# Performance work log

Hardware: AMD Instinct MI355X
Metric: run time of the kernel (lower is better)

## Reference

```python
import jax, jax.numpy as jnp
import numpy as np

IMAGE_C = 1
IMAGE_W = 28
PIXELS_PER_ROW = IMAGE_W * IMAGE_C  # 28

B, T, E = 16, IMAGE_W * IMAGE_W * IMAGE_C, 512  # T = 784
H = 8
D = E // H  # head_dim = 64


def get_2d_causal_bias(T):
    idx = jnp.arange(T)
    i = idx // PIXELS_PER_ROW          # row index
    j = (idx % PIXELS_PER_ROW) // IMAGE_C  # col index
    c = idx % IMAGE_C                  # channel index
    q_i, k_i = i[:, None], i[None, :]
    q_j, k_j = j[:, None], j[None, :]
    q_c, k_c = c[:, None], c[None, :]
    allowed = (k_i < q_i) | ((k_i == q_i) & (k_j < q_j)) | (
        (k_i == q_i) & (k_j == q_j) & (k_c <= q_c))
    bias = jnp.where(allowed, 0.0, -jnp.inf).astype(jnp.float32)
    return bias[None, None]  # [1, 1, T, T]


def setup_inputs() -> dict:
    key = jax.random.key(0)
    ks = jax.random.split(key, 5)
    s = 1.0 / np.sqrt(E)
    return {
        "x": jax.random.normal(ks[0], (B, T, E), dtype=jnp.float32),
        "Wq": jax.random.normal(ks[1], (E, E), dtype=jnp.float32) * s,
        "bq": jnp.zeros((E,), dtype=jnp.float32),
        "Wk": jax.random.normal(ks[2], (E, E), dtype=jnp.float32) * s,
        "bk": jnp.zeros((E,), dtype=jnp.float32),
        "Wv": jax.random.normal(ks[3], (E, E), dtype=jnp.float32) * s,
        "bv": jnp.zeros((E,), dtype=jnp.float32),
        "Wo": jax.random.normal(ks[4], (E, E), dtype=jnp.float32) * s,
        "bo": jnp.zeros((E,), dtype=jnp.float32),
    }


def reference(x, Wq, bq, Wk, bk, Wv, bv, Wo, bo):
    Bx, Tx, Ex = x.shape
    # projections (torch Linear: y = x @ W.T + b; here W stored as [E, E] used directly)
    Q = (x @ Wq + bq).reshape(Bx, Tx, H, D).transpose(0, 2, 1, 3)  # [B,H,T,D]
    K = (x @ Wk + bk).reshape(Bx, Tx, H, D).transpose(0, 2, 1, 3)
    V = (x @ Wv + bv).reshape(Bx, Tx, H, D).transpose(0, 2, 1, 3)
    scores = jnp.einsum("bhqd,bhkd->bhqk", Q, K) / jnp.sqrt(jnp.float32(D))
    scores = scores + get_2d_causal_bias(Tx)
    attn = jax.nn.softmax(scores, axis=-1)
    ctx = jnp.einsum("bhqk,bhkd->bhqd", attn, V)
    ctx = ctx.transpose(0, 2, 1, 3).reshape(Bx, Tx, Ex)
    return ctx @ Wo + bo
```

## Files before the change

### kernel.cpp

```cpp
#include <hip/hip_runtime.h>
#include <hip/hip_bf16.h>

#define BB    16
#define TT    784
#define TP    832
#define EE    512
#define HH    8
#define DD    64
#define BT    (BB*TT)

typedef short short8 __attribute__((ext_vector_type(8)));
typedef short short4v __attribute__((ext_vector_type(4)));
typedef float floatx4 __attribute__((ext_vector_type(4)));

__device__ __forceinline__ short f2bf(float f) {
    unsigned u = __builtin_bit_cast(unsigned, f);
    u += 0x7FFFu + ((u >> 16) & 1u);
    return (short)(u >> 16);
}

#define ASYNC16(g, l) __builtin_amdgcn_global_load_lds( \
    (const __attribute__((address_space(1))) void*)(g), \
    (__attribute__((address_space(3))) void*)(l), 16, 0, 0)

__global__ void prep_kernel(const float* __restrict__ x, short* __restrict__ xb,
                            const float* __restrict__ Wq, const float* __restrict__ Wk,
                            const float* __restrict__ Wv, short* __restrict__ wqkvt,
                            const float* __restrict__ Wo, short* __restrict__ wot,
                            short* __restrict__ Qb, short* __restrict__ Kb, short* __restrict__ Vt)
{
    __shared__ short t[64][65];
    int b = blockIdx.x;
    if (b < 3136) {
        int i = (b * 256 + threadIdx.x) * 8;
        float4 a = *(const float4*)(x + i);
        float4 c = *(const float4*)(x + i + 4);
        short8 o;
        o[0] = f2bf(a.x); o[1] = f2bf(a.y); o[2] = f2bf(a.z); o[3] = f2bf(a.w);
        o[4] = f2bf(c.x); o[5] = f2bf(c.y); o[6] = f2bf(c.z); o[7] = f2bf(c.w);
        *(short8*)(xb + i) = o;
    } else if (b < 3392) {
        const float* W; short* out; int n0, k0;
        if (b < 3328) {
            int tt = b - 3136;
            n0 = (tt % 24) * 64; k0 = (tt / 24) * 64;
            W = (n0 < 512) ? Wq : (n0 < 1024 ? Wk : Wv);
            out = wqkvt;
        } else {
            int tt = b - 3328;
            n0 = (tt % 8) * 64; k0 = (tt / 8) * 64;
            W = Wo; out = wot;
        }
        int nn0 = n0 & 511;
        for (int i = threadIdx.x; i < 4096; i += 256) {
            int r = i >> 6, c = i & 63;
            t[r][c] = f2bf(W[(k0 + r) * 512 + nn0 + c]);
        }
        __syncthreads();
        for (int i = threadIdx.x; i < 4096; i += 256) {
            int nr = i >> 6, kc = i & 63;
            out[(n0 + nr) * 512 + k0 + kc] = t[kc][nr];
        }
    } else {
        int idx = (b - 3392) * 256 + threadIdx.x;
        int d = idx & 63;
        int r = (idx >> 6) % 48;
        int bh = idx / (48 * 64);
        int off = (bh * TP + TT + r) * 64 + d;
        Qb[off] = 0; Kb[off] = 0;
        int c = idx % 48;
        int rest = idx / 48;
        int dv = rest & 63, bhv = rest >> 6;
        Vt[(bhv * 64 + dv) * TP + TT + c] = 0;
    }
}

__global__ __launch_bounds__(256, 4) void gemm_qkv_kernel(
    const short* __restrict__ A, const short* __restrict__ Bt,
    const float* __restrict__ bq, const float* __restrict__ bk, const float* __restrict__ bv,
    short* __restrict__ Qb, short* __restrict__ Kb, short* __restrict__ Vt)
{
    __shared__ __align__(16) short smem[16640];
    short* As0 = smem;
    short* Bs0 = smem + 8192;

    const int m0 = blockIdx.x * 128, n0 = blockIdx.y * 128;
    const int tid = threadIdx.x;
    const int lane = tid & 63, w = tid >> 6;
    const int wr = w >> 1, wc = w & 1;
    const int l16 = lane & 15, quad = lane >> 4;

    const short* Ag = A  + (size_t)(m0 + w * 32 + (lane >> 2)) * 512 + (lane & 3) * 8;
    const short* Bg = Bt + (size_t)(n0 + w * 32 + (lane >> 2)) * 512 + (lane & 3) * 8;
    short* Asw = As0 + (w * 32) * 32;
    short* Bsw = Bs0 + (w * 32) * 32;

    floatx4 acc[4][4];
    #pragma unroll
    for (int i = 0; i < 4; i++)
        #pragma unroll
        for (int j = 0; j < 4; j++)
            acc[i][j] = (floatx4){0.f, 0.f, 0.f, 0.f};

    ASYNC16(Ag, Asw);
    ASYNC16(Ag + 16 * 512, Asw + 16 * 32);
    ASYNC16(Bg, Bsw);
    ASYNC16(Bg + 16 * 512, Bsw + 16 * 32);

    for (int it = 0; it < 16; it++) {
        __syncthreads();
        if (it < 15) {
            int nb = (it + 1) & 1;
            int ko = (it + 1) * 32;
            ASYNC16(Ag + ko,            Asw + nb * 4096);
            ASYNC16(Ag + ko + 16 * 512, Asw + nb * 4096 + 16 * 32);
            ASYNC16(Bg + ko,            Bsw + nb * 4096);
            ASYNC16(Bg + ko + 16 * 512, Bsw + nb * 4096 + 16 * 32);
        }
        const short* as = As0 + (it & 1) * 4096;
        const short* bs = Bs0 + (it & 1) * 4096;
        short8 af[4], bf[4];
        #pragma unroll
        for (int i = 0; i < 4; i++) {
            af[i] = *(const short8*)&as[(wr * 64 + i * 16 + l16) * 32 + quad * 8];
            bf[i] = *(const short8*)&bs[(wc * 64 + i * 16 + l16) * 32 + quad * 8];
        }
        #pragma unroll
        for (int mi = 0; mi < 4; mi++)
            #pragma unroll
            for (int ni = 0; ni < 4; ni++)
                acc[mi][ni] = __builtin_amdgcn_mfma_f32_16x16x32_bf16(af[mi], bf[ni], acc[mi][ni], 0, 0, 0);
    }

    __syncthreads();

    short* Ct = smem;
    const int sel = n0 >> 9;
    const float* bias = (sel == 0) ? bq : (sel == 1) ? bk : bv;
    #pragma unroll
    for (int mi = 0; mi < 4; mi++) {
        #pragma unroll
        for (int ni = 0; ni < 4; ni++) {
            int nl = wc * 64 + ni * 16 + l16;
            int nn = (n0 + nl) & 511;
            float b = bias[nn];
            #pragma unroll
            for (int r = 0; r < 4; r++) {
                float v = acc[mi][ni][r] + b;
                if (sel == 0) v *= 0.125f;
                Ct[(wr * 64 + mi * 16 + quad * 4 + r) * 130 + nl] = f2bf(v);
            }
        }
    }
    __syncthreads();

    if (sel < 2) {
        short* dst = (sel == 0) ? Qb : Kb;
        int nl = lane * 2;
        int nn = (n0 + nl) & 511;
        int hh = nn >> 6, dd = nn & 63;
        #pragma unroll 4
        for (int rr = 0; rr < 32; rr++) {
            int ml = w * 32 + rr;
            int m = m0 + ml;
            int bb = m / TT, t = m - bb * TT;
            unsigned pv = *(const unsigned*)&Ct[ml * 130 + nl];
            *(unsigned*)&dst[((bb * HH + hh) * TP + t) * 64 + dd] = pv;
        }
    } else {
        #pragma unroll 4
        for (int rr = 0; rr < 32; rr++) {
            int nl = w * 32 + rr;
            int nn = (n0 + nl) & 511;
            int hh = nn >> 6, dd = nn & 63;
            #pragma unroll
            for (int j = 0; j < 2; j++) {
                int ml = j * 64 + lane;
                int m = m0 + ml;
                int bb = m / TT, t = m - bb * TT;
                Vt[((size_t)(bb * HH + hh) * 64 + dd) * TP + t] = Ct[ml * 130 + nl];
            }
        }
    }
}

#define LK 72
__global__ __launch_bounds__(256, 3) void attn_kernel(
    const short* __restrict__ Qb, const short* __restrict__ Kb, const short* __restrict__ Vt,
    short* __restrict__ ctx)
{
    const int g = blockIdx.x;
    const int low = g & 7, rest = g >> 3;
    const int qt = 12 - (rest >> 4);
    const int bh = ((rest & 15) << 3) | low;
    const int bb = bh >> 3, hh = bh & 7;
    const int tid = threadIdx.x;
    const int lane = tid & 63, w = tid >> 6;
    const int l16 = lane & 15, quad = lane >> 4;

    __shared__ short Ks[2][64 * LK];
    __shared__ short Vs[2][64 * LK];
    __shared__ short Ps[64 * LK];

    const int srow = tid >> 3;
    const int sc8 = (tid & 7) * 8;
    const short* Kbase = Kb + (size_t)(bh * TP) * 64;
    const short* Vbase = Vt + (size_t)(bh * 64) * TP;

    short8 kreg[2], vreg[2];
    auto load_tile = [&](int kt) {
        #pragma unroll
        for (int p = 0; p < 2; p++) {
            int row = srow + p * 32;
            kreg[p] = *(const short8*)(Kbase + (kt * 64 + row) * 64 + sc8);
            vreg[p] = *(const short8*)(Vbase + row * TP + kt * 64 + sc8);
        }
    };
    auto store_tile = [&](int b) {
        #pragma unroll
        for (int p = 0; p < 2; p++) {
            int row = srow + p * 32;
            *(short8*)&Ks[b][row * LK + sc8] = kreg[p];
            *(short8*)&Vs[b][row * LK + sc8] = vreg[p];
        }
    };

    const short* Qrow = Qb + (size_t)((bh * TP + qt * 64 + w * 16 + l16)) * 64;
    short8 qa0 = *(const short8*)(Qrow + quad * 8);
    short8 qa1 = *(const short8*)(Qrow + 32 + quad * 8);

    floatx4 accO[4];
    floatx4 accL = (floatx4){0.f, 0.f, 0.f, 0.f};
    #pragma unroll
    for (int dt = 0; dt < 4; dt++) accO[dt] = (floatx4){0.f, 0.f, 0.f, 0.f};

    short8 ones8;
    #pragma unroll
    for (int j = 0; j < 8; j++) ones8[j] = (short)0x3F80;

    const int pswz  = (quad >> 1) * 16;
    const int prswz = ((l16 >> 3) & 1) * 16;
    short* Pw = &Ps[(w * 16 + quad * 4) * LK];

    load_tile(0);
    store_tile(0);

    for (int kt = 0; kt <= qt; kt++) {
        const int cb = kt & 1;
        const bool diag = (kt == qt);
        if (kt < qt) load_tile(kt + 1);
        __syncthreads();

        float p[4][4];
        #pragma unroll
        for (int ni = 0; ni < 4; ni++) {
            if (diag && ni > w) {
                #pragma unroll
                for (int r = 0; r < 4; r++) p[ni][r] = 0.f;
                continue;
            }
            short8 kb0 = *(short8*)&Ks[cb][(ni * 16 + l16) * LK + quad * 8];
            short8 kb1 = *(short8*)&Ks[cb][(ni * 16 + l16) * LK + 32 + quad * 8];
            floatx4 z = (floatx4){0.f, 0.f, 0.f, 0.f};
            z = __builtin_amdgcn_mfma_f32_16x16x32_bf16(qa0, kb0, z, 0, 0, 0);
            z = __builtin_amdgcn_mfma_f32_16x16x32_bf16(qa1, kb1, z, 0, 0, 0);
            if (diag && ni == w) {
                #pragma unroll
                for (int r = 0; r < 4; r++)
                    if (l16 > quad * 4 + r) z[r] = -1e30f;
            }
            #pragma unroll
            for (int r = 0; r < 4; r++) p[ni][r] = __expf(z[r]);
        }

        #pragma unroll
        for (int ni = 0; ni < 4; ni++) {
            int col = (ni * 16 + l16) ^ pswz;
            #pragma unroll
            for (int r = 0; r < 4; r++)
                Pw[r * LK + col] = (short)(__builtin_bit_cast(unsigned, p[ni][r]) >> 16);
        }

        #pragma unroll
        for (int kk = 0; kk < 2; kk++) {
            if (diag && (kk * 32 > w * 16 + 15)) continue;
            short8 pa = *(short8*)&Ps[(w * 16 + l16) * LK + ((kk * 32 + quad * 8) ^ prswz)];
            accL = __builtin_amdgcn_mfma_f32_16x16x32_bf16(pa, ones8, accL, 0, 0, 0);
            #pragma unroll
            for (int dt = 0; dt < 4; dt++) {
                short8 vb = *(short8*)&Vs[cb][(dt * 16 + l16) * LK + kk * 32 + quad * 8];
                accO[dt] = __builtin_amdgcn_mfma_f32_16x16x32_bf16(pa, vb, accO[dt], 0, 0, 0);
            }
        }

        if (kt < qt) store_tile((kt + 1) & 1);
    }

    float inv_l[4];
    #pragma unroll
    for (int r = 0; r < 4; r++) inv_l[r] = 1.f / accL[r];
    #pragma unroll
    for (int dt = 0; dt < 4; dt++)
        #pragma unroll
        for (int r = 0; r < 4; r++) {
            int qg = qt * 64 + w * 16 + quad * 4 + r;
            if (qg < TT)
                ctx[(size_t)(bb * TT + qg) * 512 + hh * 64 + dt * 16 + l16] = f2bf(accO[dt][r] * inv_l[r]);
        }
}

__global__ __launch_bounds__(256, 4) void gemm_out_kernel(
    const short* __restrict__ A, const short* __restrict__ Bt,
    const float* __restrict__ bo, float* __restrict__ out)
{
    __shared__ __align__(16) short smem[16384];
    short* As0 = smem;
    short* Bs0 = smem + 8192;

    const int m0 = blockIdx.x * 128, n0 = blockIdx.y * 128;
    const int tid = threadIdx.x;
    const int lane = tid & 63, w = tid >> 6;
    const int wr = w >> 1, wc = w & 1;
    const int l16 = lane & 15, quad = lane >> 4;

    const short* Ag = A  + (size_t)(m0 + w * 32 + (lane >> 2)) * 512 + (lane & 3) * 8;
    const short* Bg = Bt + (size_t)(n0 + w * 32 + (lane >> 2)) * 512 + (lane & 3) * 8;
    short* Asw = As0 + (w * 32) * 32;
    short* Bsw = Bs0 + (w * 32) * 32;

    floatx4 acc[4][4];
    #pragma unroll
    for (int i = 0; i < 4; i++)
        #pragma unroll
        for (int j = 0; j < 4; j++)
            acc[i][j] = (floatx4){0.f, 0.f, 0.f, 0.f};

    ASYNC16(Ag, Asw);
    ASYNC16(Ag + 16 * 512, Asw + 16 * 32);
    ASYNC16(Bg, Bsw);
    ASYNC16(Bg + 16 * 512, Bsw + 16 * 32);

    for (int it = 0; it < 16; it++) {
        __syncthreads();
        if (it < 15) {
            int nb = (it + 1) & 1;
            int ko = (it + 1) * 32;
            ASYNC16(Ag + ko,            Asw + nb * 4096);
            ASYNC16(Ag + ko + 16 * 512, Asw + nb * 4096 + 16 * 32);
            ASYNC16(Bg + ko,            Bsw + nb * 4096);
            ASYNC16(Bg + ko + 16 * 512, Bsw + nb * 4096 + 16 * 32);
        }
        const short* as = As0 + (it & 1) * 4096;
        const short* bs = Bs0 + (it & 1) * 4096;
        short8 af[4], bf[4];
        #pragma unroll
        for (int i = 0; i < 4; i++) {
            af[i] = *(const short8*)&as[(wr * 64 + i * 16 + l16) * 32 + quad * 8];
            bf[i] = *(const short8*)&bs[(wc * 64 + i * 16 + l16) * 32 + quad * 8];
        }
        #pragma unroll
        for (int mi = 0; mi < 4; mi++)
            #pragma unroll
            for (int ni = 0; ni < 4; ni++)
                acc[mi][ni] = __builtin_amdgcn_mfma_f32_16x16x32_bf16(af[mi], bf[ni], acc[mi][ni], 0, 0, 0);
    }

    #pragma unroll
    for (int mi = 0; mi < 4; mi++) {
        #pragma unroll
        for (int ni = 0; ni < 4; ni++) {
            int n = n0 + wc * 64 + ni * 16 + l16;
            float bias = bo[n];
            #pragma unroll
            for (int r = 0; r < 4; r++) {
                int m = m0 + wr * 64 + mi * 16 + quad * 4 + r;
                out[(size_t)m * 512 + n] = acc[mi][ni][r] + bias;
            }
        }
    }
}

extern "C" void kernel_launch(void* const* d_in, const int* in_sizes, int n_in,
                              void* d_out, int out_size, void* d_ws, size_t ws_size,
                              hipStream_t stream) {
    const float* x  = (const float*)d_in[0];
    const float* Wq = (const float*)d_in[1];
    const float* bq = (const float*)d_in[2];
    const float* Wk = (const float*)d_in[3];
    const float* bk = (const float*)d_in[4];
    const float* Wv = (const float*)d_in[5];
    const float* bv = (const float*)d_in[6];
    const float* Wo = (const float*)d_in[7];
    const float* bo = (const float*)d_in[8];
    float* out = (float*)d_out;

    char* ws = (char*)d_ws;
    size_t off = 0;
    auto alloc = [&](size_t bytes) -> void* {
        void* p = ws + off;
        off += (bytes + 255) & ~(size_t)255;
        return p;
    };
    short* xb    = (short*)alloc((size_t)BT * EE * 2);
    short* wqkvt = (short*)alloc((size_t)1536 * 512 * 2);
    short* wot   = (short*)alloc((size_t)512 * 512 * 2);
    short* Qb    = (short*)alloc((size_t)BB * HH * TP * DD * 2);
    short* Kb    = (short*)alloc((size_t)BB * HH * TP * DD * 2);
    short* Vtb   = (short*)alloc((size_t)BB * HH * DD * TP * 2);
    short* ctxb  = (short*)alloc((size_t)BT * EE * 2);

    prep_kernel<<<4928, 256, 0, stream>>>(x, xb, Wq, Wk, Wv, wqkvt, Wo, wot, Qb, Kb, Vtb);
    gemm_qkv_kernel<<<dim3(98, 12), 256, 0, stream>>>(xb, wqkvt, bq, bk, bv, Qb, Kb, Vtb);
    attn_kernel<<<1664, 256, 0, stream>>>(Qb, Kb, Vtb, ctxb);
    gemm_out_kernel<<<dim3(98, 4), 256, 0, stream>>>(ctxb, wot, bo, out);
}
```

Measured before the change: 169.0 us.

## Use 128-row query tiles in attention and write V directly from registers

```diff
diff --git a/kernel.cpp b/kernel.cpp
--- a/kernel.cpp
+++ b/kernel.cpp
@@ -3,7 +3,8 @@
 
 #define BB    16
 #define TT    784
-#define TP    832
+#define TPK   832
+#define TPQ   896
 #define EE    512
 #define HH    8
 #define DD    64
@@ -62,16 +63,21 @@
             out[(n0 + nr) * 512 + k0 + kc] = t[kc][nr];
         }
     } else {
-        int idx = (b - 3392) * 256 + threadIdx.x;
-        int d = idx & 63;
-        int r = (idx >> 6) % 48;
-        int bh = idx / (48 * 64);
-        int off = (bh * TP + TT + r) * 64 + d;
-        Qb[off] = 0; Kb[off] = 0;
-        int c = idx % 48;
-        int rest = idx / 48;
-        int dv = rest & 63, bhv = rest >> 6;
-        Vt[(bhv * 64 + dv) * TP + TT + c] = 0;
+        int c = (b - 3392) * 256 + threadIdx.x;
+        short8 z = (short8){0,0,0,0,0,0,0,0};
+        if (c < 114688) {
+            int bh = c / 896, j = c - bh * 896;
+            *(short8*)&Qb[(bh * TPQ + TT) * 64 + j * 8] = z;
+        } else if (c < 163840) {
+            int c2 = c - 114688;
+            int bh = c2 / 384, j = c2 - bh * 384;
+            *(short8*)&Kb[(bh * TPK + TT) * 64 + j * 8] = z;
+        } else {
+            int c3 = c - 163840;
+            int bh = c3 / 384, j = c3 - bh * 384;
+            int d = j / 6, m = j - d * 6;
+            *(short8*)&Vt[(bh * 64 + d) * TPK + TT + m * 8] = z;
+        }
     }
 }
 
@@ -132,30 +138,29 @@
                 acc[mi][ni] = __builtin_amdgcn_mfma_f32_16x16x32_bf16(af[mi], bf[ni], acc[mi][ni], 0, 0, 0);
     }
 
-    __syncthreads();
-
-    short* Ct = smem;
     const int sel = n0 >> 9;
-    const float* bias = (sel == 0) ? bq : (sel == 1) ? bk : bv;
-    #pragma unroll
-    for (int mi = 0; mi < 4; mi++) {
-        #pragma unroll
-        for (int ni = 0; ni < 4; ni++) {
-            int nl = wc * 64 + ni * 16 + l16;
-            int nn = (n0 + nl) & 511;
-            float b = bias[nn];
-            #pragma unroll
-            for (int r = 0; r < 4; r++) {
-                float v = acc[mi][ni][r] + b;
-                if (sel == 0) v *= 0.125f;
-                Ct[(wr * 64 + mi * 16 + quad * 4 + r) * 130 + nl] = f2bf(v);
-            }
-        }
-    }
-    __syncthreads();
-
     if (sel < 2) {
+        __syncthreads();
+        short* Ct = smem;
+        const float* bias = (sel == 0) ? bq : bk;
+        #pragma unroll
+        for (int mi = 0; mi < 4; mi++) {
+            #pragma unroll
+            for (int ni = 0; ni < 4; ni++) {
+                int nl = wc * 64 + ni * 16 + l16;
+                int nn = (n0 + nl) & 511;
+                float b = bias[nn];
+                #pragma unroll
+                for (int r = 0; r < 4; r++) {
+                    float v = acc[mi][ni][r] + b;
+                    if (sel == 0) v *= 0.125f;
+                    Ct[(wr * 64 + mi * 16 + quad * 4 + r) * 130 + nl] = f2bf(v);
+                }
+            }
+        }
+        __syncthreads();
         short* dst = (sel == 0) ? Qb : Kb;
+        const int tp = (sel == 0) ? TPQ : TPK;
         int nl = lane * 2;
         int nn = (n0 + nl) & 511;
         int hh = nn >> 6, dd = nn & 63;
@@ -165,34 +170,35 @@
             int m = m0 + ml;
             int bb = m / TT, t = m - bb * TT;
             unsigned pv = *(const unsigned*)&Ct[ml * 130 + nl];
-            *(unsigned*)&dst[((bb * HH + hh) * TP + t) * 64 + dd] = pv;
+            *(unsigned*)&dst[((bb * HH + hh) * tp + t) * 64 + dd] = pv;
         }
     } else {
-        #pragma unroll 4
-        for (int rr = 0; rr < 32; rr++) {
-            int nl = w * 32 + rr;
-            int nn = (n0 + nl) & 511;
-            int hh = nn >> 6, dd = nn & 63;
-            #pragma unroll
-            for (int j = 0; j < 2; j++) {
-                int ml = j * 64 + lane;
-                int m = m0 + ml;
-                int bb = m / TT, t = m - bb * TT;
-                Vt[((size_t)(bb * HH + hh) * 64 + dd) * TP + t] = Ct[ml * 130 + nl];
+        #pragma unroll
+        for (int mi = 0; mi < 4; mi++) {
+            int m = m0 + wr * 64 + mi * 16 + quad * 4;
+            int bb = m / TT, t = m - bb * TT;
+            #pragma unroll
+            for (int ni = 0; ni < 4; ni++) {
+                int nn = (n0 + wc * 64 + ni * 16 + l16) & 511;
+                int hh = nn >> 6, dd = nn & 63;
+                float b = bv[nn];
+                short4v pv;
+                #pragma unroll
+                for (int r = 0; r < 4; r++) pv[r] = f2bf(acc[mi][ni][r] + b);
+                *(short4v*)&Vt[((size_t)(bb * HH + hh) * 64 + dd) * TPK + t] = pv;
             }
         }
     }
 }
 
 #define LK 72
-__global__ __launch_bounds__(256, 3) void attn_kernel(
+__global__ __launch_bounds__(256, 2) void attn_kernel(
     const short* __restrict__ Qb, const short* __restrict__ Kb, const short* __restrict__ Vt,
     short* __restrict__ ctx)
 {
     const int g = blockIdx.x;
-    const int low = g & 7, rest = g >> 3;
-    const int qt = 12 - (rest >> 4);
-    const int bh = ((rest & 15) << 3) | low;
+    const int qt = 6 - (g >> 7);
+    const int bh = g & 127;
     const int bb = bh >> 3, hh = bh & 7;
     const int tid = threadIdx.x;
     const int lane = tid & 63, w = tid >> 6;
@@ -200,12 +206,12 @@
 
     __shared__ short Ks[2][64 * LK];
     __shared__ short Vs[2][64 * LK];
-    __shared__ short Ps[64 * LK];
+    __shared__ short Ps[128 * LK];
 
     const int srow = tid >> 3;
     const int sc8 = (tid & 7) * 8;
-    const short* Kbase = Kb + (size_t)(bh * TP) * 64;
-    const short* Vbase = Vt + (size_t)(bh * 64) * TP;
+    const short* Kbase = Kb + (size_t)(bh * TPK) * 64;
+    const short* Vbase = Vt + (size_t)(bh * 64) * TPK;
 
     short8 kreg[2], vreg[2];
     auto load_tile = [&](int kt) {
@@ -213,7 +219,7 @@
         for (int p = 0; p < 2; p++) {
             int row = srow + p * 32;
             kreg[p] = *(const short8*)(Kbase + (kt * 64 + row) * 64 + sc8);
-            vreg[p] = *(const short8*)(Vbase + row * TP + kt * 64 + sc8);
+            vreg[p] = *(const short8*)(Vbase + row * TPK + kt * 64 + sc8);
         }
     };
     auto store_tile = [&](int b) {
@@ -225,14 +231,23 @@
         }
     };
 
-    const short* Qrow = Qb + (size_t)((bh * TP + qt * 64 + w * 16 + l16)) * 64;
-    short8 qa0 = *(const short8*)(Qrow + quad * 8);
-    short8 qa1 = *(const short8*)(Qrow + 32 + quad * 8);
-
-    floatx4 accO[4];
-    floatx4 accL = (floatx4){0.f, 0.f, 0.f, 0.f};
-    #pragma unroll
-    for (int dt = 0; dt < 4; dt++) accO[dt] = (floatx4){0.f, 0.f, 0.f, 0.f};
+    const int q0 = qt * 128;
+    short8 qa[2][2];
+    #pragma unroll
+    for (int mi = 0; mi < 2; mi++) {
+        const short* Qrow = Qb + (size_t)(bh * TPQ + q0 + w * 32 + mi * 16 + l16) * 64;
+        qa[mi][0] = *(const short8*)(Qrow + quad * 8);
+        qa[mi][1] = *(const short8*)(Qrow + 32 + quad * 8);
+    }
+
+    floatx4 accO[2][4];
+    floatx4 accL[2];
+    #pragma unroll
+    for (int mi = 0; mi < 2; mi++) {
+        accL[mi] = (floatx4){0.f, 0.f, 0.f, 0.f};
+        #pragma unroll
+        for (int dt = 0; dt < 4; dt++) accO[mi][dt] = (floatx4){0.f, 0.f, 0.f, 0.f};
+    }
 
     short8 ones8;
     #pragma unroll
@@ -240,73 +255,89 @@
 
     const int pswz  = (quad >> 1) * 16;
     const int prswz = ((l16 >> 3) & 1) * 16;
-    short* Pw = &Ps[(w * 16 + quad * 4) * LK];
+
+    const int kt_end = (2 * qt + 2 < 13) ? (2 * qt + 2) : 13;
 
     load_tile(0);
     store_tile(0);
 
-    for (int kt = 0; kt <= qt; kt++) {
+    for (int kt = 0; kt < kt_end; kt++) {
         const int cb = kt & 1;
-        const bool diag = (kt == qt);
-        if (kt < qt) load_tile(kt + 1);
-        __syncthreads();
-
-        float p[4][4];
-        #pragma unroll
-        for (int ni = 0; ni < 4; ni++) {
-            if (diag && ni > w) {
+        if (kt + 1 < kt_end) load_tile(kt + 1);
+        __syncthreads();
+
+        #pragma unroll
+        for (int mi = 0; mi < 2; mi++) {
+            const int qr0 = q0 + w * 32 + mi * 16;
+            float p[4][4];
+            #pragma unroll
+            for (int ni = 0; ni < 4; ni++) {
+                const int kbase = kt * 64 + ni * 16;
+                if (kbase > qr0 + 15) {
+                    #pragma unroll
+                    for (int r = 0; r < 4; r++) p[ni][r] = 0.f;
+                    continue;
+                }
+                short8 kb0 = *(short8*)&Ks[cb][(ni * 16 + l16) * LK + quad * 8];
+                short8 kb1 = *(short8*)&Ks[cb][(ni * 16 + l16) * LK + 32 + quad * 8];
+                floatx4 z = (floatx4){0.f, 0.f, 0.f, 0.f};
+                z = __builtin_amdgcn_mfma_f32_16x16x32_bf16(qa[mi][0], kb0, z, 0, 0, 0);
+                z = __builtin_amdgcn_mfma_f32_16x16x32_bf16(qa[mi][1], kb1, z, 0, 0, 0);
+                if (kbase == qr0) {
+                    #pragma unroll
+                    for (int r = 0; r < 4; r++)
+                        if (l16 > quad * 4 + r) z[r] = -1e30f;
+                }
                 #pragma unroll
-                for (int r = 0; r < 4; r++) p[ni][r] = 0.f;
-                continue;
-            }
-            short8 kb0 = *(short8*)&Ks[cb][(ni * 16 + l16) * LK + quad * 8];
-            short8 kb1 = *(short8*)&Ks[cb][(ni * 16 + l16) * LK + 32 + quad * 8];
-            floatx4 z = (floatx4){0.f, 0.f, 0.f, 0.f};
-            z = __builtin_amdgcn_mfma_f32_16x16x32_bf16(qa0, kb0, z, 0, 0, 0);
-            z = __builtin_amdgcn_mfma_f32_16x16x32_bf16(qa1, kb1, z, 0, 0, 0);
-            if (diag && ni == w) {
+                for (int r = 0; r < 4; r++) p[ni][r] = __expf(z[r]);
+            }
+            short* Pw = &Ps[(w * 32 + mi * 16 + quad * 4) * LK];
+            #pragma unroll
+            for (int ni = 0; ni < 4; ni++) {
+                int col = (ni * 16 + l16) ^ pswz;
                 #pragma unroll
                 for (int r = 0; r < 4; r++)
-                    if (l16 > quad * 4 + r) z[r] = -1e30f;
-            }
-            #pragma unroll
-            for (int r = 0; r < 4; r++) p[ni][r] = __expf(z[r]);
-        }
-
-        #pragma unroll
-        for (int ni = 0; ni < 4; ni++) {
-            int col = (ni * 16 + l16) ^ pswz;
-            #pragma unroll
-            for (int r = 0; r < 4; r++)
-                Pw[r * LK + col] = (short)(__builtin_bit_cast(unsigned, p[ni][r]) >> 16);
+                    Pw[r * LK + col] = (short)(__builtin_bit_cast(unsigned, p[ni][r]) >> 16);
+            }
         }
 
         #pragma unroll
         for (int kk = 0; kk < 2; kk++) {
-            if (diag && (kk * 32 > w * 16 + 15)) continue;
-            short8 pa = *(short8*)&Ps[(w * 16 + l16) * LK + ((kk * 32 + quad * 8) ^ prswz)];
-            accL = __builtin_amdgcn_mfma_f32_16x16x32_bf16(pa, ones8, accL, 0, 0, 0);
-            #pragma unroll
-            for (int dt = 0; dt < 4; dt++) {
-                short8 vb = *(short8*)&Vs[cb][(dt * 16 + l16) * LK + kk * 32 + quad * 8];
-                accO[dt] = __builtin_amdgcn_mfma_f32_16x16x32_bf16(pa, vb, accO[dt], 0, 0, 0);
-            }
-        }
-
-        if (kt < qt) store_tile((kt + 1) & 1);
-    }
-
-    float inv_l[4];
-    #pragma unroll
-    for (int r = 0; r < 4; r++) inv_l[r] = 1.f / accL[r];
-    #pragma unroll
-    for (int dt = 0; dt < 4; dt++)
-        #pragma unroll
-        for (int r = 0; r < 4; r++) {
-            int qg = qt * 64 + w * 16 + quad * 4 + r;
-            if (qg < TT)
-                ctx[(size_t)(bb * TT + qg) * 512 + hh * 64 + dt * 16 + l16] = f2bf(accO[dt][r] * inv_l[r]);
-        }
+            const int kb32 = kt * 64 + kk * 32;
+            if (kb32 > q0 + w * 32 + 31) continue;
+            short8 vb[4];
+            #pragma unroll
+            for (int dt = 0; dt < 4; dt++)
+                vb[dt] = *(short8*)&Vs[cb][(dt * 16 + l16) * LK + kk * 32 + quad * 8];
+            #pragma unroll
+            for (int mi = 0; mi < 2; mi++) {
+                if (kb32 > q0 + w * 32 + mi * 16 + 15) continue;
+                short8 pa = *(short8*)&Ps[(w * 32 + mi * 16 + l16) * LK + ((kk * 32 + quad * 8) ^ prswz)];
+                accL[mi] = __builtin_amdgcn_mfma_f32_16x16x32_bf16(pa, ones8, accL[mi], 0, 0, 0);
+                #pragma unroll
+                for (int dt = 0; dt < 4; dt++)
+                    accO[mi][dt] = __builtin_amdgcn_mfma_f32_16x16x32_bf16(pa, vb[dt], accO[mi][dt], 0, 0, 0);
+            }
+        }
+
+        if (kt + 1 < kt_end) store_tile((kt + 1) & 1);
+    }
+
+    #pragma unroll
+    for (int mi = 0; mi < 2; mi++) {
+        float inv_l[4];
+        #pragma unroll
+        for (int r = 0; r < 4; r++) inv_l[r] = 1.f / accL[mi][r];
+        #pragma unroll
+        for (int dt = 0; dt < 4; dt++)
+            #pragma unroll
+            for (int r = 0; r < 4; r++) {
+                int qg = q0 + w * 32 + mi * 16 + quad * 4 + r;
+                if (qg < TT)
+                    ctx[(size_t)(bb * TT + qg) * 512 + hh * 64 + dt * 16 + l16] =
+                        f2bf(accO[mi][dt][r] * inv_l[r]);
+            }
+    }
 }
 
 __global__ __launch_bounds__(256, 4) void gemm_out_kernel(
@@ -404,13 +435,13 @@
     short* xb    = (short*)alloc((size_t)BT * EE * 2);
     short* wqkvt = (short*)alloc((size_t)1536 * 512 * 2);
     short* wot   = (short*)alloc((size_t)512 * 512 * 2);
-    short* Qb    = (short*)alloc((size_t)BB * HH * TP * DD * 2);
-    short* Kb    = (short*)alloc((size_t)BB * HH * TP * DD * 2);
-    short* Vtb   = (short*)alloc((size_t)BB * HH * DD * TP * 2);
+    short* Qb    = (short*)alloc((size_t)BB * HH * TPQ * DD * 2);
+    short* Kb    = (short*)alloc((size_t)BB * HH * TPK * DD * 2);
+    short* Vtb   = (short*)alloc((size_t)BB * HH * DD * TPK * 2);
     short* ctxb  = (short*)alloc((size_t)BT * EE * 2);
 
-    prep_kernel<<<4928, 256, 0, stream>>>(x, xb, Wq, Wk, Wv, wqkvt, Wo, wot, Qb, Kb, Vtb);
+    prep_kernel<<<4224, 256, 0, stream>>>(x, xb, Wq, Wk, Wv, wqkvt, Wo, wot, Qb, Kb, Vtb);
     gemm_qkv_kernel<<<dim3(98, 12), 256, 0, stream>>>(xb, wqkvt, bq, bk, bv, Qb, Kb, Vtb);
-    attn_kernel<<<1664, 256, 0, stream>>>(Qb, Kb, Vtb, ctxb);
+    attn_kernel<<<896, 256, 0, stream>>>(Qb, Kb, Vtb, ctxb);
     gemm_out_kernel<<<dim3(98, 4), 256, 0, stream>>>(ctxb, wot, bo, out);
 }
```

New measurement: 175.4 us. 3.8% more time.

## Enlarge QKV GEMM tile to 256x128 and write V directly without staging

Applied to the files above, without the earlier changes.

```diff
diff --git a/kernel.cpp b/kernel.cpp
--- a/kernel.cpp
+++ b/kernel.cpp
@@ -3,7 +3,8 @@
 
 #define BB    16
 #define TT    784
-#define TP    832
+#define TPK   832
+#define TPQ   896
 #define EE    512
 #define HH    8
 #define DD    64
@@ -62,123 +63,136 @@
             out[(n0 + nr) * 512 + k0 + kc] = t[kc][nr];
         }
     } else {
-        int idx = (b - 3392) * 256 + threadIdx.x;
-        int d = idx & 63;
-        int r = (idx >> 6) % 48;
-        int bh = idx / (48 * 64);
-        int off = (bh * TP + TT + r) * 64 + d;
-        Qb[off] = 0; Kb[off] = 0;
-        int c = idx % 48;
-        int rest = idx / 48;
-        int dv = rest & 63, bhv = rest >> 6;
-        Vt[(bhv * 64 + dv) * TP + TT + c] = 0;
-    }
-}
-
-__global__ __launch_bounds__(256, 4) void gemm_qkv_kernel(
+        int c = (b - 3392) * 256 + threadIdx.x;
+        short8 z = (short8){0,0,0,0,0,0,0,0};
+        if (c < 114688) {
+            int bh = c / 896, j = c - bh * 896;
+            *(short8*)&Qb[(bh * TPQ + TT) * 64 + j * 8] = z;
+        } else if (c < 163840) {
+            int c2 = c - 114688;
+            int bh = c2 / 384, j = c2 - bh * 384;
+            *(short8*)&Kb[(bh * TPK + TT) * 64 + j * 8] = z;
+        } else {
+            int c3 = c - 163840;
+            int bh = c3 / 384, j = c3 - bh * 384;
+            int d = j / 6, m = j - d * 6;
+            *(short8*)&Vt[(bh * 64 + d) * TPK + TT + m * 8] = z;
+        }
+    }
+}
+
+__global__ __launch_bounds__(256, 2) void gemm_qkv_kernel(
     const short* __restrict__ A, const short* __restrict__ Bt,
     const float* __restrict__ bq, const float* __restrict__ bk, const float* __restrict__ bv,
     short* __restrict__ Qb, short* __restrict__ Kb, short* __restrict__ Vt)
 {
-    __shared__ __align__(16) short smem[16640];
+    __shared__ __align__(16) short smem[24576];
     short* As0 = smem;
-    short* Bs0 = smem + 8192;
-
-    const int m0 = blockIdx.x * 128, n0 = blockIdx.y * 128;
+    short* Bs0 = smem + 16384;
+
+    const int m0 = blockIdx.x * 256, n0 = blockIdx.y * 128;
     const int tid = threadIdx.x;
     const int lane = tid & 63, w = tid >> 6;
-    const int wr = w >> 1, wc = w & 1;
     const int l16 = lane & 15, quad = lane >> 4;
 
-    const short* Ag = A  + (size_t)(m0 + w * 32 + (lane >> 2)) * 512 + (lane & 3) * 8;
+    const short* Ag = A  + (size_t)(m0 + w * 64 + (lane >> 2)) * 512 + (lane & 3) * 8;
     const short* Bg = Bt + (size_t)(n0 + w * 32 + (lane >> 2)) * 512 + (lane & 3) * 8;
-    short* Asw = As0 + (w * 32) * 32;
-    short* Bsw = Bs0 + (w * 32) * 32;
-
-    floatx4 acc[4][4];
+    short* Asw = As0 + w * 64 * 32;
+    short* Bsw = Bs0 + w * 32 * 32;
+
+    floatx4 acc[4][8];
     #pragma unroll
     for (int i = 0; i < 4; i++)
         #pragma unroll
-        for (int j = 0; j < 4; j++)
+        for (int j = 0; j < 8; j++)
             acc[i][j] = (floatx4){0.f, 0.f, 0.f, 0.f};
 
-    ASYNC16(Ag, Asw);
-    ASYNC16(Ag + 16 * 512, Asw + 16 * 32);
+    #pragma unroll
+    for (int p = 0; p < 4; p++) ASYNC16(Ag + p * 16 * 512, Asw + p * 512);
     ASYNC16(Bg, Bsw);
-    ASYNC16(Bg + 16 * 512, Bsw + 16 * 32);
+    ASYNC16(Bg + 16 * 512, Bsw + 512);
 
     for (int it = 0; it < 16; it++) {
         __syncthreads();
         if (it < 15) {
             int nb = (it + 1) & 1;
             int ko = (it + 1) * 32;
-            ASYNC16(Ag + ko,            Asw + nb * 4096);
-            ASYNC16(Ag + ko + 16 * 512, Asw + nb * 4096 + 16 * 32);
+            #pragma unroll
+            for (int p = 0; p < 4; p++)
+                ASYNC16(Ag + ko + p * 16 * 512, Asw + nb * 8192 + p * 512);
             ASYNC16(Bg + ko,            Bsw + nb * 4096);
-            ASYNC16(Bg + ko + 16 * 512, Bsw + nb * 4096 + 16 * 32);
-        }
-        const short* as = As0 + (it & 1) * 4096;
+            ASYNC16(Bg + ko + 16 * 512, Bsw + nb * 4096 + 512);
+        }
+        const short* as = As0 + (it & 1) * 8192;
         const short* bs = Bs0 + (it & 1) * 4096;
-        short8 af[4], bf[4];
-        #pragma unroll
-        for (int i = 0; i < 4; i++) {
-            af[i] = *(const short8*)&as[(wr * 64 + i * 16 + l16) * 32 + quad * 8];
-            bf[i] = *(const short8*)&bs[(wc * 64 + i * 16 + l16) * 32 + quad * 8];
-        }
+        short8 af[4], bf[8];
+        #pragma unroll
+        for (int i = 0; i < 4; i++)
+            af[i] = *(const short8*)&as[(w * 64 + i * 16 + l16) * 32 + quad * 8];
+        #pragma unroll
+        for (int j = 0; j < 8; j++)
+            bf[j] = *(const short8*)&bs[(j * 16 + l16) * 32 + quad * 8];
         #pragma unroll
         for (int mi = 0; mi < 4; mi++)
             #pragma unroll
-            for (int ni = 0; ni < 4; ni++)
+            for (int ni = 0; ni < 8; ni++)
                 acc[mi][ni] = __builtin_amdgcn_mfma_f32_16x16x32_bf16(af[mi], bf[ni], acc[mi][ni], 0, 0, 0);
     }
 
-    __syncthreads();
-
-    short* Ct = smem;
     const int sel = n0 >> 9;
-    const float* bias = (sel == 0) ? bq : (sel == 1) ? bk : bv;
-    #pragma unroll
-    for (int mi = 0; mi < 4; mi++) {
-        #pragma unroll
-        for (int ni = 0; ni < 4; ni++) {
-            int nl = wc * 64 + ni * 16 + l16;
-            int nn = (n0 + nl) & 511;
-            float b = bias[nn];
-            #pragma unroll
-            for (int r = 0; r < 4; r++) {
-                float v = acc[mi][ni][r] + b;
-                if (sel == 0) v *= 0.125f;
-                Ct[(wr * 64 + mi * 16 + quad * 4 + r) * 130 + nl] = f2bf(v);
-            }
-        }
-    }
-    __syncthreads();
-
-    if (sel < 2) {
+    if (sel == 2) {
+        #pragma unroll
+        for (int mi = 0; mi < 4; mi++) {
+            int m = m0 + w * 64 + mi * 16 + quad * 4;
+            int bb = m / TT, t = m - bb * TT;
+            #pragma unroll
+            for (int ni = 0; ni < 8; ni++) {
+                int nn = (n0 + ni * 16 + l16) & 511;
+                int hh = nn >> 6, dd = nn & 63;
+                float b = bv[nn];
+                short4v pv;
+                #pragma unroll
+                for (int r = 0; r < 4; r++) pv[r] = f2bf(acc[mi][ni][r] + b);
+                *(short4v*)&Vt[((size_t)(bb * HH + hh) * 64 + dd) * TPK + t] = pv;
+            }
+        }
+    } else {
+        short* Ct = smem;
+        const float* bias = (sel == 0) ? bq : bk;
         short* dst = (sel == 0) ? Qb : Kb;
-        int nl = lane * 2;
-        int nn = (n0 + nl) & 511;
-        int hh = nn >> 6, dd = nn & 63;
-        #pragma unroll 4
-        for (int rr = 0; rr < 32; rr++) {
-            int ml = w * 32 + rr;
-            int m = m0 + ml;
-            int bb = m / TT, t = m - bb * TT;
-            unsigned pv = *(const unsigned*)&Ct[ml * 130 + nl];
-            *(unsigned*)&dst[((bb * HH + hh) * TP + t) * 64 + dd] = pv;
-        }
-    } else {
-        #pragma unroll 4
-        for (int rr = 0; rr < 32; rr++) {
-            int nl = w * 32 + rr;
-            int nn = (n0 + nl) & 511;
-            int hh = nn >> 6, dd = nn & 63;
-            #pragma unroll
-            for (int j = 0; j < 2; j++) {
-                int ml = j * 64 + lane;
-                int m = m0 + ml;
+        const int tp = (sel == 0) ? TPQ : TPK;
+        const int nlc = lane * 2;
+        const int nnc = (n0 + nlc) & 511;
+        const int hhc = nnc >> 6, ddc = nnc & 63;
+        #pragma unroll
+        for (int h = 0; h < 2; h++) {
+            __syncthreads();
+            if ((w >> 1) == h) {
+                int wl = w & 1;
+                #pragma unroll
+                for (int mi = 0; mi < 4; mi++) {
+                    #pragma unroll
+                    for (int ni = 0; ni < 8; ni++) {
+                        int nl = ni * 16 + l16;
+                        int nn = (n0 + nl) & 511;
+                        float b = bias[nn];
+                        #pragma unroll
+                        for (int r = 0; r < 4; r++) {
+                            float v = acc[mi][ni][r] + b;
+                            if (sel == 0) v *= 0.125f;
+                            Ct[(wl * 64 + mi * 16 + quad * 4 + r) * 130 + nl] = f2bf(v);
+                        }
+                    }
+                }
+            }
+            __syncthreads();
+            #pragma unroll 4
+            for (int rr = 0; rr < 32; rr++) {
+                int ml = w * 32 + rr;
+                int m = m0 + h * 128 + ml;
                 int bb = m / TT, t = m - bb * TT;
-                Vt[((size_t)(bb * HH + hh) * 64 + dd) * TP + t] = Ct[ml * 130 + nl];
+                unsigned pv = *(const unsigned*)&Ct[ml * 130 + nlc];
+                *(unsigned*)&dst[((bb * HH + hhc) * tp + t) * 64 + ddc] = pv;
             }
         }
     }
@@ -204,8 +218,8 @@
 
     const int srow = tid >> 3;
     const int sc8 = (tid & 7) * 8;
-    const short* Kbase = Kb + (size_t)(bh * TP) * 64;
-    const short* Vbase = Vt + (size_t)(bh * 64) * TP;
+    const short* Kbase = Kb + (size_t)(bh * TPK) * 64;
+    const short* Vbase = Vt + (size_t)(bh * 64) * TPK;
 
     short8 kreg[2], vreg[2];
     auto load_tile = [&](int kt) {
@@ -213,7 +227,7 @@
         for (int p = 0; p < 2; p++) {
             int row = srow + p * 32;
             kreg[p] = *(const short8*)(Kbase + (kt * 64 + row) * 64 + sc8);
-            vreg[p] = *(const short8*)(Vbase + row * TP + kt * 64 + sc8);
+            vreg[p] = *(const short8*)(Vbase + row * TPK + kt * 64 + sc8);
         }
     };
     auto store_tile = [&](int b) {
@@ -225,7 +239,7 @@
         }
     };
 
-    const short* Qrow = Qb + (size_t)((bh * TP + qt * 64 + w * 16 + l16)) * 64;
+    const short* Qrow = Qb + (size_t)(bh * TPQ + qt * 64 + w * 16 + l16) * 64;
     short8 qa0 = *(const short8*)(Qrow + quad * 8);
     short8 qa1 = *(const short8*)(Qrow + 32 + quad * 8);
 
@@ -404,13 +418,13 @@
     short* xb    = (short*)alloc((size_t)BT * EE * 2);
     short* wqkvt = (short*)alloc((size_t)1536 * 512 * 2);
     short* wot   = (short*)alloc((size_t)512 * 512 * 2);
-    short* Qb    = (short*)alloc((size_t)BB * HH * TP * DD * 2);
-    short* Kb    = (short*)alloc((size_t)BB * HH * TP * DD * 2);
-    short* Vtb   = (short*)alloc((size_t)BB * HH * DD * TP * 2);
+    short* Qb    = (short*)alloc((size_t)BB * HH * TPQ * DD * 2);
+    short* Kb    = (short*)alloc((size_t)BB * HH * TPK * DD * 2);
+    short* Vtb   = (short*)alloc((size_t)BB * HH * DD * TPK * 2);
     short* ctxb  = (short*)alloc((size_t)BT * EE * 2);
 
-    prep_kernel<<<4928, 256, 0, stream>>>(x, xb, Wq, Wk, Wv, wqkvt, Wo, wot, Qb, Kb, Vtb);
-    gemm_qkv_kernel<<<dim3(98, 12), 256, 0, stream>>>(xb, wqkvt, bq, bk, bv, Qb, Kb, Vtb);
+    prep_kernel<<<4224, 256, 0, stream>>>(x, xb, Wq, Wk, Wv, wqkvt, Wo, wot, Qb, Kb, Vtb);
+    gemm_qkv_kernel<<<dim3(49, 12), 256, 0, stream>>>(xb, wqkvt, bq, bk, bv, Qb, Kb, Vtb);
     attn_kernel<<<1664, 256, 0, stream>>>(Qb, Kb, Vtb, ctxb);
     gemm_out_kernel<<<dim3(98, 4), 256, 0, stream>>>(ctxb, wot, bo, out);
 }
```

Result: slower. 172.6 us (+2.1%).
